# Kernel optimization log

Hardware: AMD Instinct MI355X
Metric: run time of the kernel (lower is better)

The kernel has to match this reference:

```python
import jax, jax.numpy as jnp
import numpy as np
import math

B, S, D, H = 8, 1024, 1024, 16
HD = D // H  # head_features = 64
SCALE = math.sqrt(HD)


def setup_inputs() -> dict:
    key = jax.random.key(0)
    k0, k1, k2, k3, k4 = jax.random.split(key, 5)
    x = jax.random.normal(k0, (B, S, D), dtype=jnp.float32)
    attn_mask = (jax.random.uniform(k1, (B, S, S)) < 0.9).astype(jnp.float32)
    w_scale = 1.0 / math.sqrt(D)  # keep unsafe exp in finite range
    Wq = jax.random.normal(k2, (D, D), dtype=jnp.float32) * w_scale
    Wk = jax.random.normal(k3, (D, D), dtype=jnp.float32) * w_scale
    Wv = jax.random.normal(k4, (D, D), dtype=jnp.float32) * w_scale
    return {"x": x, "attn_mask": attn_mask, "Wq": Wq, "Wk": Wk, "Wv": Wv}


def reference(x, attn_mask, Wq, Wk, Wv):
    b, s, _ = x.shape

    def split_heads(t):  # [b,s,D] -> [b,H,s,HD]
        return t.reshape(b, s, H, HD).transpose(0, 2, 1, 3)

    q = split_heads(x @ Wq)
    k = split_heads(x @ Wk)
    v = split_heads(x @ Wv)

    # unsafe softmax: exp without max subtraction, multiplicative mask, +1e-8 denom
    scores = jnp.einsum('bhsd,bhtd->bhst', q, k) / SCALE
    e = jnp.exp(scores) * attn_mask[:, None, :, :]
    w = e / (e.sum(axis=3, keepdims=True) + 1e-8)

    ctx = jnp.einsum('bhst,bhtd->bhsd', w, v)  # [b,H,s,HD]
    return ctx.transpose(0, 2, 1, 3).reshape(b, s, D)
```

## Files before the change

kernel.cpp:

```cpp
#include <hip/hip_runtime.h>

#define KDIM 1024

typedef _Float16 half8 __attribute__((ext_vector_type(8)));
typedef _Float16 half4 __attribute__((ext_vector_type(4)));
typedef __fp16 fp16x2 __attribute__((ext_vector_type(2)));
typedef __fp16 fp16x4 __attribute__((ext_vector_type(4)));
typedef float f32x4 __attribute__((ext_vector_type(4)));

#if defined(__has_builtin)
#if __has_builtin(__builtin_amdgcn_global_load_lds)
#define HAVE_GLDS 1
#endif
#if __has_builtin(__builtin_amdgcn_exp2f)
#define EXP2(x) __builtin_amdgcn_exp2f(x)
#endif
#if __has_builtin(__builtin_amdgcn_cvt_pkrtz)
#define HAVE_PKRTZ 1
#endif
#if __has_builtin(__builtin_amdgcn_fdot2)
#define HAVE_FDOT2 1
#endif
#endif
#ifndef EXP2
#define EXP2(x) exp2f(x)
#endif

__device__ __forceinline__ void stage16(const _Float16* g, _Float16* wave_base, int lane) {
#ifdef HAVE_GLDS
  __builtin_amdgcn_global_load_lds(
      (const __attribute__((address_space(1))) void*)g,
      (__attribute__((address_space(3))) void*)wave_base, 16, 0, 0);
#else
  *(half8*)(wave_base + lane * 8) = *(const half8*)g;
#endif
}

#define BARRIER() __builtin_amdgcn_s_barrier()
#define LGKM0()                                         \
  do {                                                  \
    asm volatile("s_waitcnt lgkmcnt(0)" ::: "memory");  \
    __builtin_amdgcn_sched_barrier(0);                  \
  } while (0)
#define VMCNT(n)                                               \
  do {                                                         \
    asm volatile("s_waitcnt vmcnt(" #n ")" ::: "memory");      \
  } while (0)

__global__ void prep_kernel(const float* __restrict__ x, const float* __restrict__ am,
                            const float* __restrict__ Wq, const float* __restrict__ Wk,
                            const float* __restrict__ Wv, _Float16* __restrict__ xb,
                            _Float16* __restrict__ Wqkvt, unsigned long long* __restrict__ bits) {
  __shared__ _Float16 tile[32][33];
  int bid = blockIdx.x;
  if (bid < 8192) {
    size_t i = ((size_t)bid * 256 + threadIdx.x) * 4;
    float4 v = *(const float4*)(x + i);
    half4 h = { (_Float16)v.x, (_Float16)v.y, (_Float16)v.z, (_Float16)v.w };
    *(half4*)(xb + i) = h;
  } else if (bid < 11264) {
    int zz = bid - 8192;
    int z = zz >> 10;
    int rem = zz & 1023;
    int bx = rem & 31, by = rem >> 5;
    const float* src = z == 0 ? Wq : (z == 1 ? Wk : Wv);
    _Float16* dst = Wqkvt + (size_t)z * KDIM * KDIM;
    float sc = (z == 0) ? 0.18033688011112042f : 1.0f;
    int tx = threadIdx.x & 31, ty = threadIdx.x >> 5;
    int c0 = bx * 32, r0 = by * 32;
#pragma unroll
    for (int i = 0; i < 4; i++) {
      int r = r0 + ty + i * 8;
      tile[tx][ty + i * 8] = (_Float16)(src[(size_t)r * KDIM + c0 + tx] * sc);
    }
    __syncthreads();
#pragma unroll
    for (int i = 0; i < 4; i++) {
      int n = c0 + ty + i * 8;
      dst[(size_t)n * KDIM + r0 + tx] = tile[ty + i * 8][tx];
    }
  } else {
    size_t i = (size_t)(bid - 11264) * 256 + threadIdx.x;
    unsigned long long b = __ballot(am[i] != 0.0f);
    if ((threadIdx.x & 63) == 0) bits[i >> 6] = b;
  }
}

template <int MH, int NH>
__device__ __forceinline__ void mfma_quad(f32x4 (&acc)[8][4], const half8 (&af)[4][2],
                                          const half8 (&bf)[2][2]) {
  __builtin_amdgcn_s_setprio(1);
#pragma unroll
  for (int mi = 0; mi < 4; ++mi)
#pragma unroll
    for (int nj = 0; nj < 2; ++nj) {
      acc[MH * 4 + mi][NH * 2 + nj] = __builtin_amdgcn_mfma_f32_16x16x32_f16(
          af[mi][0], bf[nj][0], acc[MH * 4 + mi][NH * 2 + nj], 0, 0, 0);
      acc[MH * 4 + mi][NH * 2 + nj] = __builtin_amdgcn_mfma_f32_16x16x32_f16(
          af[mi][1], bf[nj][1], acc[MH * 4 + mi][NH * 2 + nj], 0, 0, 0);
    }
  __builtin_amdgcn_s_setprio(0);
}

__global__ __launch_bounds__(512, 2)
void gemm_kernel(const _Float16* __restrict__ A, const _Float16* __restrict__ Bt,
                 _Float16* __restrict__ Qt, _Float16* __restrict__ Kh,
                 _Float16* __restrict__ Vth) {
  __shared__ _Float16 As[2 * 16384];
  __shared__ _Float16 Bs[2 * 16384];
  int tid = threadIdx.x;
  int lane = tid & 63, w = tid >> 6;
  int la = lane & 15, qd = lane >> 4;
  int wm = w & 1, wn = w >> 1;
  int bid = blockIdx.x;
  int wg = (bid & 7) * 48 + (bid >> 3);
  int by = wg / 12, bx = wg - by * 12;
  int m0 = by * 256, n0 = bx * 256;
  int srow = tid >> 3;
  int scc = ((srow & 7) ^ (tid & 7)) << 3;
  const int rc0 = ((qd ^ (la & 7)) << 3);
  const int rc1 = (((4 | qd) ^ (la & 7)) << 3);

  const _Float16* Ab = A + (size_t)m0 * KDIM;
  const _Float16* Bb = Bt + (size_t)n0 * KDIM;

  auto stA = [&](int buf, int h, int kt) {
#pragma unroll
    for (int l = 0; l < 2; ++l) {
      int r = h * 128 + srow + l * 64;
      stage16(Ab + (size_t)r * KDIM + kt + scc,
              As + buf * 16384 + h * 8192 + l * 4096 + w * 512, lane);
    }
  };
  auto stB = [&](int buf, int h, int kt) {
#pragma unroll
    for (int l = 0; l < 2; ++l) {
      int r = h * 128 + srow + l * 64;
      stage16(Bb + (size_t)r * KDIM + kt + scc,
              Bs + buf * 16384 + h * 8192 + l * 4096 + w * 512, lane);
    }
  };

  f32x4 acc[8][4] = {};
  half8 af[4][2], bf[2][2];

  auto ldAf = [&](int buf, int mh) {
#pragma unroll
    for (int mi = 0; mi < 4; ++mi) {
      const _Float16* p = As + buf * 16384 + mh * 8192 + (wm * 64 + mi * 16 + la) * 64;
      af[mi][0] = *(const half8*)(p + rc0);
      af[mi][1] = *(const half8*)(p + rc1);
    }
  };
  auto ldBf = [&](int buf, int nh) {
#pragma unroll
    for (int nj = 0; nj < 2; ++nj) {
      const _Float16* p = Bs + buf * 16384 + nh * 8192 + (wn * 32 + nj * 16 + la) * 64;
      bf[nj][0] = *(const half8*)(p + rc0);
      bf[nj][1] = *(const half8*)(p + rc1);
    }
  };

  stA(0, 0, 0); stA(0, 1, 0); stB(0, 0, 0); stB(0, 1, 0);
  stA(1, 0, 64); stB(1, 0, 64);
  VMCNT(4);
  BARRIER();

  for (int t = 0; t < 16; ++t) {
    int cur = t & 1, nxt = cur ^ 1;
    int k1 = (t + 1) << 6, k2 = (t + 2) << 6;
    ldAf(cur, 0);
    ldBf(cur, 0);
    if (t < 15) stA(nxt, 1, k1);
    BARRIER();
    LGKM0();
    mfma_quad<0, 0>(acc, af, bf);
    BARRIER();
    ldBf(cur, 1);
    if (t < 15) stB(nxt, 1, k1);
    BARRIER();
    LGKM0();
    mfma_quad<0, 1>(acc, af, bf);
    BARRIER();
    ldAf(cur, 1);
    ldBf(cur, 0);
    if (t < 14) stA(cur, 0, k2);
    BARRIER();
    LGKM0();
    mfma_quad<1, 0>(acc, af, bf);
    BARRIER();
    ldBf(cur, 1);
    if (t < 14) stB(cur, 0, k2);
    BARRIER();
    LGKM0();
    mfma_quad<1, 1>(acc, af, bf);
    if (t < 14) { VMCNT(4); } else { VMCNT(0); }
    BARRIER();
  }

  int which = n0 >> 10;
  int n0k = n0 & 1023;
  if (which == 1) {
#pragma unroll
    for (int mh = 0; mh < 2; ++mh) {
      int srow0 = m0 + mh * 128 + wm * 64;
      int b = srow0 >> 10, s0 = srow0 & 1023;
#pragma unroll
      for (int nh = 0; nh < 2; ++nh)
#pragma unroll
        for (int nj = 0; nj < 2; ++nj) {
          int colh = n0k + nh * 128 + wn * 32 + nj * 16;
          int hh = colh >> 6;
          int d = (colh & 63) + la;
          _Float16* kb = Kh + (size_t)(b * 16 + hh) * 1024 * 64;
#pragma unroll
          for (int mi = 0; mi < 4; ++mi) {
            f32x4 v = acc[mh * 4 + mi][nh * 2 + nj];
            int s = s0 + mi * 16 + qd * 4;
#pragma unroll
            for (int rg = 0; rg < 4; ++rg)
              kb[(size_t)(s + rg) * 64 + d] = (_Float16)v[rg];
          }
        }
    }
  } else {
    _Float16* dst = (which == 0) ? Qt : Vth;
    _Float16* ep = As + w * 1280;
    int rr = lane >> 2, c4 = lane & 3;
#pragma unroll
    for (int mh = 0; mh < 2; ++mh) {
      int srow0 = m0 + mh * 128 + wm * 64;
      int b = srow0 >> 10, s0 = srow0 & 1023;
#pragma unroll
      for (int nh = 0; nh < 2; ++nh)
#pragma unroll
        for (int nj = 0; nj < 2; ++nj) {
          int colh = n0k + nh * 128 + wn * 32 + nj * 16;
          int hh = colh >> 6, d0 = colh & 63;
#pragma unroll
          for (int mi = 0; mi < 4; ++mi) {
            f32x4 v = acc[mh * 4 + mi][nh * 2 + nj];
            half4 hv = { (_Float16)v[0], (_Float16)v[1], (_Float16)v[2], (_Float16)v[3] };
            *(half4*)(ep + la * 72 + mi * 16 + qd * 4) = hv;
          }
          half8 o0 = *(const half8*)(ep + rr * 72 + c4 * 16);
          half8 o1 = *(const half8*)(ep + rr * 72 + c4 * 16 + 8);
          _Float16* gp = dst + ((size_t)(b * 16 + hh) * 64 + d0 + rr) * 1024 + s0 + c4 * 16;
          *(half8*)gp = o0;
          *(half8*)(gp + 8) = o1;
        }
    }
  }
}

__global__ __launch_bounds__(512, 2)
void attn_kernel(const _Float16* __restrict__ Qt, const _Float16* __restrict__ K,
                 const _Float16* __restrict__ Vt, const unsigned long long* __restrict__ mbits,
                 float* __restrict__ out) {
  __shared__ _Float16 Ks[2][2 * 64 * 32];
  __shared__ _Float16 Vs[2][2 * 64 * 40];
  int tid = threadIdx.x;
  int lane = tid & 63, w4 = tid >> 6;
  int la = lane & 15, qd = lane >> 4;
  int linear = blockIdx.x;
  int xlo = linear & 7;
  int tmp = linear >> 3;
  int qt = tmp & 3;
  int hb = (tmp >> 2) * 8 + xlo;
  int h = hb & 15, b = hb >> 4;
  const _Float16* Qp = Qt + (size_t)hb * 64 * 1024;
  const _Float16* Kp = K + (size_t)hb * 1024 * 64;
  const _Float16* Vp = Vt + (size_t)hb * 64 * 1024;
  int q0w = qt * 256 + w4 * 16;
  half8 qf[2][2];
#pragma unroll
  for (int qi = 0; qi < 2; qi++)
#pragma unroll
    for (int ks = 0; ks < 2; ks++)
#pragma unroll
      for (int j = 0; j < 8; j++)
        qf[qi][ks][j] = Qp[(size_t)(ks * 32 + qd * 8 + j) * 1024 + q0w + qi * 128 + la];
  unsigned long long mq[2][4];
#pragma unroll
  for (int qi = 0; qi < 2; qi++) {
    const ulonglong2* mp =
        (const ulonglong2*)(mbits + ((size_t)b * 1024 + q0w + qi * 128 + la) * 16 + qd * 4);
    ulonglong2 m01 = mp[0];
    ulonglong2 m23 = mp[1];
    mq[qi][0] = m01.x; mq[qi][1] = m01.y; mq[qi][2] = m23.x; mq[qi][3] = m23.y;
  }
  f32x4 acco[2][4] = {};
  float rs[2] = {0.f, 0.f};
  int kt_t = (tid & 255) >> 2;
  int kt_d = (tid >> 8) * 32 + (tid & 3) * 8;
  int vd = tid >> 3;
  int vt = (tid & 7) * 8;
  int vs_off = (vt >= 32 ? 2560 : 0) + vd * 40 + (vt & 31);
#if defined(HAVE_FDOT2) && defined(HAVE_PKRTZ)
  fp16x2 one2 = { (__fp16)1.0f, (__fp16)1.0f };
#endif
  {
    stage16(Kp + (size_t)kt_t * 64 + kt_d, Ks[0] + w4 * 512, lane);
    half8 vv = *(const half8*)(Vp + (size_t)vd * 1024 + vt);
    *(half8*)(Vs[0] + vs_off) = vv;
  }
  __syncthreads();
  for (int tt = 0; tt < 16; tt++) {
    int cur = tt & 1, nxt = cur ^ 1;
    half8 vvn;
    if (tt < 15) {
      vvn = *(const half8*)(Vp + (size_t)vd * 1024 + (tt + 1) * 64 + vt);
      stage16(Kp + (size_t)((tt + 1) * 64 + kt_t) * 64 + kt_d, Ks[nxt] + w4 * 512, lane);
    }
    const _Float16* ks_ = Ks[cur];
    const _Float16* vs_ = Vs[cur];
    unsigned long long mw0 = __shfl(mq[0][tt & 3], ((tt >> 2) << 4) + la);
    unsigned long long mw1 = __shfl(mq[1][tt & 3], ((tt >> 2) << 4) + la);
#pragma unroll
    for (int tsub = 0; tsub < 4; tsub++) {
      half8 kf0 = *(const half8*)(ks_ + (tsub * 16 + la) * 32 + qd * 8);
      half8 kf1 = *(const half8*)(ks_ + 2048 + (tsub * 16 + la) * 32 + qd * 8);
      f32x4 a0 = {}, a1 = {};
      a0 = __builtin_amdgcn_mfma_f32_16x16x32_f16(kf0, qf[0][0], a0, 0, 0, 0);
      a1 = __builtin_amdgcn_mfma_f32_16x16x32_f16(kf0, qf[1][0], a1, 0, 0, 0);
      a0 = __builtin_amdgcn_mfma_f32_16x16x32_f16(kf1, qf[0][1], a0, 0, 0, 0);
      a1 = __builtin_amdgcn_mfma_f32_16x16x32_f16(kf1, qf[1][1], a1, 0, 0, 0);
      half4 pf[2];
#pragma unroll
      for (int qi = 0; qi < 2; qi++) {
        const f32x4& aa = qi ? a1 : a0;
        unsigned long long mw = qi ? mw1 : mw0;
        float e0 = ((mw >> (tsub * 16 + qd * 4 + 0)) & 1ull) ? EXP2(aa[0]) : 0.0f;
        float e1 = ((mw >> (tsub * 16 + qd * 4 + 1)) & 1ull) ? EXP2(aa[1]) : 0.0f;
        float e2 = ((mw >> (tsub * 16 + qd * 4 + 2)) & 1ull) ? EXP2(aa[2]) : 0.0f;
        float e3 = ((mw >> (tsub * 16 + qd * 4 + 3)) & 1ull) ? EXP2(aa[3]) : 0.0f;
#ifdef HAVE_PKRTZ
        fp16x2 p01 = __builtin_amdgcn_cvt_pkrtz(e0, e1);
        fp16x2 p23 = __builtin_amdgcn_cvt_pkrtz(e2, e3);
        fp16x4 pfv = __builtin_shufflevector(p01, p23, 0, 1, 2, 3);
        pf[qi] = __builtin_bit_cast(half4, pfv);
#else
        pf[qi][0] = (_Float16)e0; pf[qi][1] = (_Float16)e1;
        pf[qi][2] = (_Float16)e2; pf[qi][3] = (_Float16)e3;
#endif
#if defined(HAVE_FDOT2) && defined(HAVE_PKRTZ)
        rs[qi] = __builtin_amdgcn_fdot2(p01, one2, rs[qi], false);
        rs[qi] = __builtin_amdgcn_fdot2(p23, one2, rs[qi], false);
#else
        rs[qi] += e0 + e1 + e2 + e3;
#endif
      }
#pragma unroll
      for (int nsub = 0; nsub < 4; nsub++) {
        half4 vf = *(const half4*)(vs_ + (tsub >> 1) * 2560 + (nsub * 16 + la) * 40 +
                                   (tsub & 1) * 16 + qd * 4);
        acco[0][nsub] = __builtin_amdgcn_mfma_f32_16x16x16f16(pf[0], vf, acco[0][nsub], 0, 0, 0);
        acco[1][nsub] = __builtin_amdgcn_mfma_f32_16x16x16f16(pf[1], vf, acco[1][nsub], 0, 0, 0);
      }
    }
    if (tt < 15) *(half8*)(Vs[nxt] + vs_off) = vvn;
    __syncthreads();
  }
  float* op = out + (size_t)b * 1024 * 1024 + (size_t)h * 64;
#pragma unroll
  for (int qi = 0; qi < 2; qi++) {
    float r0 = rs[qi];
    r0 += __shfl_xor(r0, 16);
    r0 += __shfl_xor(r0, 32);
    float inv_q = 1.0f / (r0 + 1e-8f);
#pragma unroll
    for (int rg = 0; rg < 4; rg++) {
      float inv = __shfl(inv_q, qd * 4 + rg);
      int s = q0w + qi * 128 + qd * 4 + rg;
#pragma unroll
      for (int nsub = 0; nsub < 4; nsub++)
        op[(size_t)s * 1024 + nsub * 16 + la] = acco[qi][nsub][rg] * inv;
    }
  }
}

extern "C" void kernel_launch(void* const* d_in, const int* in_sizes, int n_in,
                              void* d_out, int out_size, void* d_ws, size_t ws_size,
                              hipStream_t stream) {
  (void)in_sizes; (void)n_in; (void)out_size; (void)ws_size;
  const float* x = (const float*)d_in[0];
  const float* am = (const float*)d_in[1];
  const float* Wq = (const float*)d_in[2];
  const float* Wk = (const float*)d_in[3];
  const float* Wv = (const float*)d_in[4];
  float* out = (float*)d_out;

  char* p = (char*)d_ws;
  _Float16* xb = (_Float16*)p;    p += (size_t)8192 * 1024 * 2;
  _Float16* Wqkvt = (_Float16*)p; p += (size_t)3 * 1024 * 1024 * 2;
  _Float16* Qt = (_Float16*)p;    p += (size_t)8192 * 1024 * 2;
  _Float16* Kh = (_Float16*)p;    p += (size_t)8192 * 1024 * 2;
  _Float16* Vth = (_Float16*)p;   p += (size_t)8192 * 1024 * 2;
  unsigned long long* mb = (unsigned long long*)p;

  prep_kernel<<<44032, 256, 0, stream>>>(x, am, Wq, Wk, Wv, xb, Wqkvt, mb);
  gemm_kernel<<<dim3(384), 512, 0, stream>>>(xb, Wqkvt, Qt, Kh, Vth);
  attn_kernel<<<512, 512, 0, stream>>>(Qt, Kh, Vth, mb, out);
}
```

Measured before the change: 259.6 us.

## Restructure GEMM main loop with double B fragments and deeper prefetch

New measurement: 253.7 us. 2.3% less time.

```diff
diff --git a/kernel.cpp b/kernel.cpp
--- a/kernel.cpp
+++ b/kernel.cpp
@@ -86,22 +86,6 @@
   }
 }
 
-template <int MH, int NH>
-__device__ __forceinline__ void mfma_quad(f32x4 (&acc)[8][4], const half8 (&af)[4][2],
-                                          const half8 (&bf)[2][2]) {
-  __builtin_amdgcn_s_setprio(1);
-#pragma unroll
-  for (int mi = 0; mi < 4; ++mi)
-#pragma unroll
-    for (int nj = 0; nj < 2; ++nj) {
-      acc[MH * 4 + mi][NH * 2 + nj] = __builtin_amdgcn_mfma_f32_16x16x32_f16(
-          af[mi][0], bf[nj][0], acc[MH * 4 + mi][NH * 2 + nj], 0, 0, 0);
-      acc[MH * 4 + mi][NH * 2 + nj] = __builtin_amdgcn_mfma_f32_16x16x32_f16(
-          af[mi][1], bf[nj][1], acc[MH * 4 + mi][NH * 2 + nj], 0, 0, 0);
-    }
-  __builtin_amdgcn_s_setprio(0);
-}
-
 __global__ __launch_bounds__(512, 2)
 void gemm_kernel(const _Float16* __restrict__ A, const _Float16* __restrict__ Bt,
                  _Float16* __restrict__ Qt, _Float16* __restrict__ Kh,
@@ -124,79 +108,142 @@
   const _Float16* Ab = A + (size_t)m0 * KDIM;
   const _Float16* Bb = Bt + (size_t)n0 * KDIM;
 
-  auto stA = [&](int buf, int h, int kt) {
-#pragma unroll
-    for (int l = 0; l < 2; ++l) {
-      int r = h * 128 + srow + l * 64;
-      stage16(Ab + (size_t)r * KDIM + kt + scc,
-              As + buf * 16384 + h * 8192 + l * 4096 + w * 512, lane);
-    }
-  };
-  auto stB = [&](int buf, int h, int kt) {
-#pragma unroll
-    for (int l = 0; l < 2; ++l) {
-      int r = h * 128 + srow + l * 64;
-      stage16(Bb + (size_t)r * KDIM + kt + scc,
-              Bs + buf * 16384 + h * 8192 + l * 4096 + w * 512, lane);
-    }
-  };
+  const _Float16* pA0a = Ab + (size_t)(srow) * KDIM + scc;
+  const _Float16* pA0b = Ab + (size_t)(srow + 64) * KDIM + scc;
+  const _Float16* pA1a = Ab + (size_t)(srow + 128) * KDIM + scc;
+  const _Float16* pA1b = Ab + (size_t)(srow + 192) * KDIM + scc;
+  const _Float16* pB0a = Bb + (size_t)(srow) * KDIM + scc;
+  const _Float16* pB0b = Bb + (size_t)(srow + 64) * KDIM + scc;
+  const _Float16* pB1a = Bb + (size_t)(srow + 128) * KDIM + scc;
+  const _Float16* pB1b = Bb + (size_t)(srow + 192) * KDIM + scc;
+
+  _Float16* ldsAw = As + w * 512;
+  _Float16* ldsBw = Bs + w * 512;
+
+  const _Float16* baseA0 = As + wm * 4096 + la * 64 + rc0;
+  const _Float16* baseA1 = As + wm * 4096 + la * 64 + rc1;
+  const _Float16* baseB0 = Bs + wn * 2048 + la * 64 + rc0;
+  const _Float16* baseB1 = Bs + wn * 2048 + la * 64 + rc1;
 
   f32x4 acc[8][4] = {};
-  half8 af[4][2], bf[2][2];
-
-  auto ldAf = [&](int buf, int mh) {
-#pragma unroll
-    for (int mi = 0; mi < 4; ++mi) {
-      const _Float16* p = As + buf * 16384 + mh * 8192 + (wm * 64 + mi * 16 + la) * 64;
-      af[mi][0] = *(const half8*)(p + rc0);
-      af[mi][1] = *(const half8*)(p + rc1);
-    }
-  };
-  auto ldBf = [&](int buf, int nh) {
-#pragma unroll
-    for (int nj = 0; nj < 2; ++nj) {
-      const _Float16* p = Bs + buf * 16384 + nh * 8192 + (wn * 32 + nj * 16 + la) * 64;
-      bf[nj][0] = *(const half8*)(p + rc0);
-      bf[nj][1] = *(const half8*)(p + rc1);
-    }
-  };
-
-  stA(0, 0, 0); stA(0, 1, 0); stB(0, 0, 0); stB(0, 1, 0);
-  stA(1, 0, 64); stB(1, 0, 64);
-  VMCNT(4);
+  half8 af[4][2], bf0[2][2], bf1[2][2];
+
+#define STAGE_A1(NXT)                                              \
+  do {                                                             \
+    stage16(pA1a, ldsAw + (NXT) * 16384 + 8192, lane);             \
+    stage16(pA1b, ldsAw + (NXT) * 16384 + 8192 + 4096, lane);      \
+    pA1a += 64; pA1b += 64;                                        \
+  } while (0)
+#define STAGE_B1(NXT)                                              \
+  do {                                                             \
+    stage16(pB1a, ldsBw + (NXT) * 16384 + 8192, lane);             \
+    stage16(pB1b, ldsBw + (NXT) * 16384 + 8192 + 4096, lane);      \
+    pB1a += 64; pB1b += 64;                                        \
+  } while (0)
+#define STAGE_A0(CUR)                                              \
+  do {                                                             \
+    stage16(pA0a, ldsAw + (CUR) * 16384, lane);                    \
+    stage16(pA0b, ldsAw + (CUR) * 16384 + 4096, lane);             \
+    pA0a += 64; pA0b += 64;                                        \
+  } while (0)
+#define STAGE_B0(CUR)                                              \
+  do {                                                             \
+    stage16(pB0a, ldsBw + (CUR) * 16384, lane);                    \
+    stage16(pB0b, ldsBw + (CUR) * 16384 + 4096, lane);             \
+    pB0a += 64; pB0b += 64;                                        \
+  } while (0)
+#define LD_AF(CUR, MH)                                                              \
+  do {                                                                              \
+    _Pragma("unroll") for (int mi = 0; mi < 4; ++mi) {                              \
+      af[mi][0] = *(const half8*)(baseA0 + (CUR) * 16384 + (MH) * 8192 + mi * 1024); \
+      af[mi][1] = *(const half8*)(baseA1 + (CUR) * 16384 + (MH) * 8192 + mi * 1024); \
+    }                                                                               \
+  } while (0)
+#define LD_BF(BF, CUR, NH)                                                          \
+  do {                                                                              \
+    _Pragma("unroll") for (int nj = 0; nj < 2; ++nj) {                              \
+      BF[nj][0] = *(const half8*)(baseB0 + (CUR) * 16384 + (NH) * 8192 + nj * 1024); \
+      BF[nj][1] = *(const half8*)(baseB1 + (CUR) * 16384 + (NH) * 8192 + nj * 1024); \
+    }                                                                               \
+  } while (0)
+#define MFMA_Q(MH, NH, BF)                                                          \
+  do {                                                                              \
+    __builtin_amdgcn_s_setprio(1);                                                  \
+    _Pragma("unroll") for (int mi = 0; mi < 4; ++mi)                                \
+        _Pragma("unroll") for (int nj = 0; nj < 2; ++nj) {                          \
+      acc[(MH) * 4 + mi][(NH) * 2 + nj] = __builtin_amdgcn_mfma_f32_16x16x32_f16(   \
+          af[mi][0], BF[nj][0], acc[(MH) * 4 + mi][(NH) * 2 + nj], 0, 0, 0);        \
+      acc[(MH) * 4 + mi][(NH) * 2 + nj] = __builtin_amdgcn_mfma_f32_16x16x32_f16(   \
+          af[mi][1], BF[nj][1], acc[(MH) * 4 + mi][(NH) * 2 + nj], 0, 0, 0);        \
+    }                                                                               \
+    __builtin_amdgcn_s_setprio(0);                                                  \
+  } while (0)
+
+  stage16(pA0a, ldsAw, lane);
+  stage16(pA0b, ldsAw + 4096, lane);
+  stage16(pB0a, ldsBw, lane);
+  stage16(pB0b, ldsBw + 4096, lane);
+  stage16(pA1a, ldsAw + 8192, lane);
+  stage16(pA1b, ldsAw + 8192 + 4096, lane);
+  stage16(pB1a, ldsBw + 8192, lane);
+  stage16(pB1b, ldsBw + 8192 + 4096, lane);
+  stage16(pA0a + 64, ldsAw + 16384, lane);
+  stage16(pA0b + 64, ldsAw + 16384 + 4096, lane);
+  stage16(pB0a + 64, ldsBw + 16384, lane);
+  stage16(pB0b + 64, ldsBw + 16384 + 4096, lane);
+  pA0a += 128; pA0b += 128; pB0a += 128; pB0b += 128;
+  pA1a += 64;  pA1b += 64;  pB1a += 64;  pB1b += 64;
+  VMCNT(8);
   BARRIER();
 
-  for (int t = 0; t < 16; ++t) {
-    int cur = t & 1, nxt = cur ^ 1;
-    int k1 = (t + 1) << 6, k2 = (t + 2) << 6;
-    ldAf(cur, 0);
-    ldBf(cur, 0);
-    if (t < 15) stA(nxt, 1, k1);
-    BARRIER();
-    LGKM0();
-    mfma_quad<0, 0>(acc, af, bf);
-    BARRIER();
-    ldBf(cur, 1);
-    if (t < 15) stB(nxt, 1, k1);
-    BARRIER();
-    LGKM0();
-    mfma_quad<0, 1>(acc, af, bf);
-    BARRIER();
-    ldAf(cur, 1);
-    ldBf(cur, 0);
-    if (t < 14) stA(cur, 0, k2);
-    BARRIER();
-    LGKM0();
-    mfma_quad<1, 0>(acc, af, bf);
-    BARRIER();
-    ldBf(cur, 1);
-    if (t < 14) stB(cur, 0, k2);
-    BARRIER();
-    LGKM0();
-    mfma_quad<1, 1>(acc, af, bf);
-    if (t < 14) { VMCNT(4); } else { VMCNT(0); }
-    BARRIER();
-  }
+#define KTILE(T, CUR, NXT)                                     \
+  do {                                                         \
+    int t = (T);                                               \
+                                                  \
+    LD_AF(CUR, 0);                                             \
+    LD_BF(bf0, CUR, 0);                                        \
+    if (t < 15) STAGE_A1(NXT);                                 \
+    BARRIER();                                                 \
+    LGKM0();                                                   \
+    MFMA_Q(0, 0, bf0);                                         \
+    if (t < 15) { VMCNT(6); } else { VMCNT(0); }               \
+    BARRIER();                                                 \
+                                                  \
+    LD_BF(bf1, CUR, 1);                                        \
+    if (t < 15) STAGE_B1(NXT);                                 \
+    BARRIER();                                                 \
+    LGKM0();                                                   \
+    MFMA_Q(0, 1, bf1);                                         \
+    BARRIER();                                                 \
+                                                  \
+    LD_AF(CUR, 1);                                             \
+    if (t < 14) STAGE_A0(CUR);                                 \
+    BARRIER();                                                 \
+    LGKM0();                                                   \
+    MFMA_Q(1, 0, bf0);                                         \
+    BARRIER();                                                 \
+                                                  \
+    if (t < 14) STAGE_B0(CUR);                                 \
+    BARRIER();                                                 \
+    MFMA_Q(1, 1, bf1);                                         \
+    if (t < 14) { VMCNT(8); } else if (t == 14) { VMCNT(4); }  \
+    BARRIER();                                                 \
+  } while (0)
+
+#pragma unroll 1
+  for (int tp = 0; tp < 8; ++tp) {
+    KTILE(2 * tp, 0, 1);
+    KTILE(2 * tp + 1, 1, 0);
+  }
+
+#undef KTILE
+#undef MFMA_Q
+#undef LD_BF
+#undef LD_AF
+#undef STAGE_B0
+#undef STAGE_A0
+#undef STAGE_B1
+#undef STAGE_A1
 
   int which = n0 >> 10;
   int n0k = n0 & 1023;
```
